# Kernel tuning notes

Hardware: AMD Instinct MI355X
Metric: run time of the kernel (lower is better)

## Reference

```python
import jax, jax.numpy as jnp
import numpy as np

H = 150  # hidden per direction

def _lstm_dir(x, w_ih, w_hh, b_ih, b_hh):
    # x: [B, T, D] -> hs: [B, T, H]; PyTorch gate order i,f,g,o
    B = x.shape[0]
    xg = jnp.einsum('btd,gd->btg', x, w_ih) + b_ih + b_hh  # precompute input projection [B,T,4H]
    def step(carry, xt):
        h, c = carry
        g = xt + h @ w_hh.T
        i, f, gg, o = jnp.split(g, 4, axis=-1)
        i, f, o = jax.nn.sigmoid(i), jax.nn.sigmoid(f), jax.nn.sigmoid(o)
        c = f * c + i * jnp.tanh(gg)
        h = o * jnp.tanh(c)
        return (h, c), h
    init = (jnp.zeros((B, H), x.dtype), jnp.zeros((B, H), x.dtype))
    _, hs = jax.lax.scan(step, init, jnp.swapaxes(xg, 0, 1))  # [T,B,H]
    return jnp.swapaxes(hs, 0, 1)

def _bilstm(x, w_ih_f, w_hh_f, b_ih_f, b_hh_f, w_ih_b, w_hh_b, b_ih_b, b_hh_b):
    fwd = _lstm_dir(x, w_ih_f, w_hh_f, b_ih_f, b_hh_f)
    bwd = jnp.flip(_lstm_dir(jnp.flip(x, axis=1), w_ih_b, w_hh_b, b_ih_b, b_hh_b), axis=1)
    return jnp.concatenate([fwd, bwd], axis=-1)  # [B, T, 2H]

def setup_inputs() -> dict:
    key = jax.random.key(0)
    ks = jax.random.split(key, 20)
    s = 0.05
    d = {
        'sentences': jax.random.normal(ks[0], (1024, 128, 343), jnp.float32),
        'w_ih_f1': jax.random.normal(ks[1], (600, 343)) * s,
        'w_hh_f1': jax.random.normal(ks[2], (600, 150)) * s,
        'b_ih_f1': jax.random.normal(ks[3], (600,)) * s,
        'b_hh_f1': jax.random.normal(ks[4], (600,)) * s,
        'w_ih_b1': jax.random.normal(ks[5], (600, 343)) * s,
        'w_hh_b1': jax.random.normal(ks[6], (600, 150)) * s,
        'b_ih_b1': jax.random.normal(ks[7], (600,)) * s,
        'b_hh_b1': jax.random.normal(ks[8], (600,)) * s,
        'w_ih_f2': jax.random.normal(ks[9], (600, 300)) * s,
        'w_hh_f2': jax.random.normal(ks[10], (600, 150)) * s,
        'b_ih_f2': jax.random.normal(ks[11], (600,)) * s,
        'b_hh_f2': jax.random.normal(ks[12], (600,)) * s,
        'w_ih_b2': jax.random.normal(ks[13], (600, 300)) * s,
        'w_hh_b2': jax.random.normal(ks[14], (600, 150)) * s,
        'b_ih_b2': jax.random.normal(ks[15], (600,)) * s,
        'b_hh_b2': jax.random.normal(ks[16], (600,)) * s,
        'w_out': jax.random.normal(ks[17], (7, 300)) * s,
        'b_out': jax.random.normal(ks[18], (7,)) * s,
    }
    return d

def reference(sentences, w_ih_f1, w_hh_f1, b_ih_f1, b_hh_f1, w_ih_b1, w_hh_b1, b_ih_b1, b_hh_b1,
              w_ih_f2, w_hh_f2, b_ih_f2, b_hh_f2, w_ih_b2, w_hh_b2, b_ih_b2, b_hh_b2, w_out, b_out):
    # Layer 1: per-sentence BiLSTM over words, batched instead of a python loop (dropout is eval-mode identity)
    word_out = _bilstm(sentences, w_ih_f1, w_hh_f1, b_ih_f1, b_hh_f1, w_ih_b1, w_hh_b1, b_ih_b1, b_hh_b1)  # [S,T,300]
    sent_emb = jnp.max(word_out, axis=1)  # max-pool over words -> [S,300]
    # Layer 2: BiLSTM over the sequence of sentence embeddings (batch of 1 paragraph)
    sent_out = _bilstm(sent_emb[None], w_ih_f2, w_hh_f2, b_ih_f2, b_hh_f2, w_ih_b2, w_hh_b2, b_ih_b2, b_hh_b2)[0]  # [S,300]
    log_probs = jax.nn.log_softmax(sent_out @ w_out.T + b_out, axis=-1)  # [S,7]
    return log_probs
```

## Files before the change

kernel.cpp:

```cpp
#include <hip/hip_runtime.h>
#include <hip/hip_bf16.h>
#include <hip/hip_fp16.h>

typedef short bf16x8 __attribute__((ext_vector_type(8)));
typedef float f32x4 __attribute__((ext_vector_type(4)));
typedef unsigned short u16x4 __attribute__((ext_vector_type(4)));
typedef unsigned int uint32;

#define MFMA_B16(a,b,c) __builtin_amdgcn_mfma_f32_16x16x32_bf16(a,b,c,0,0,0)

#define NS   1024
#define TLEN 128
#define DD   343
#define HH   150
#define GG   600
#define KX   352
#define KXP  44
#define KHP  20
#define NP   640

#define OFF_WXP  0u
#define OFF_WHP  901120u
#define OFF_B1   1310720u
#define OFF_W2B  1315840u
#define OFF_W2I  1725440u
#define OFF_SE   3184640u
#define OFF_XG2  4413440u
#define OFF_H2O  9328640u
#define OFF_XBF  10557440u
#define NEED_BF  102832128ull

#define PE0 450560
#define PE1 655360
#define PE2 656640
#define PE3 861440
#define PE4 1226240

__device__ __forceinline__ float rcp_fast(float x) { return __builtin_amdgcn_rcpf(x); }
__device__ __forceinline__ float sigm(float x) { return rcp_fast(1.f + __expf(-x)); }
__device__ __forceinline__ float tanh_fast(float x) { return 1.f - 2.f * rcp_fast(__expf(2.f * x) + 1.f); }

typedef __attribute__((address_space(1))) const void GASV;
typedef __attribute__((address_space(3))) void LASV;
__device__ __forceinline__ void gload_lds16(const void* g, void* l) {
  __builtin_amdgcn_global_load_lds((GASV*)g, (LASV*)l, 16, 0, 0);
}

__device__ __forceinline__ void bar_lds() {
  asm volatile("s_waitcnt lgkmcnt(0)" ::: "memory");
  __builtin_amdgcn_s_barrier();
  asm volatile("" ::: "memory");
}
__device__ __forceinline__ void bar_full() {
  asm volatile("s_waitcnt vmcnt(0) lgkmcnt(0)" ::: "memory");
  __builtin_amdgcn_s_barrier();
  asm volatile("" ::: "memory");
}

__device__ __forceinline__ unsigned short f2bu(float v) {
  __hip_bfloat16 b = __float2bfloat16(v);
  return __builtin_bit_cast(unsigned short, b);
}

__global__ __launch_bounds__(256) void prep_kernel(
    const float* __restrict__ wif1, const float* __restrict__ whf1,
    const float* __restrict__ bif1, const float* __restrict__ bhf1,
    const float* __restrict__ wib1, const float* __restrict__ whb1,
    const float* __restrict__ bib1, const float* __restrict__ bhb1,
    const float* __restrict__ wif2, const float* __restrict__ wib2,
    const float* __restrict__ whf2, const float* __restrict__ whb2,
    __hip_bfloat16* __restrict__ WXp, __hip_bfloat16* __restrict__ WHp,
    float* __restrict__ B1, __hip_bfloat16* __restrict__ W2B, float* __restrict__ W2I)
{
  int i = blockIdx.x * 256 + threadIdx.x;
  if (i < PE0) {
    int d = i / 225280; int r = i - d * 225280;
    int p = r / 5120;   int r2 = r - p * 5120;
    int n = r2 >> 3;    int j = r2 & 7;
    int k = p * 8 + j;
    const float* w = d ? wib1 : wif1;
    float v = (n < GG && k < DD) ? w[n * DD + k] : 0.f;
    WXp[i] = __float2bfloat16(v);
  } else if (i < PE1) {
    int ii = i - PE0;
    int d = ii / 102400; int r = ii - d * 102400;
    int p = r / 5120;    int r2 = r - p * 5120;
    int n = r2 >> 3;     int j = r2 & 7;
    int k = p * 8 + j;
    const float* w = d ? whb1 : whf1;
    float v = (n < GG && k < HH) ? w[n * HH + k] : 0.f;
    WHp[ii] = __float2bfloat16(v);
  } else if (i < PE2) {
    int ii = i - PE1;
    int d = ii / NP; int n = ii - d * NP;
    float v = 0.f;
    if (n < GG) v = d ? (bib1[n] + bhb1[n]) : (bif1[n] + bhf1[n]);
    B1[ii] = v;
  } else if (i < PE3) {
    int ii = i - PE2;
    int d = ii / 102400; int r = ii - d * 102400;
    int n = r / 160;     int k = r - n * 160;
    const float* w = d ? whb2 : whf2;
    float v = (n < GG && k < HH) ? w[n * HH + k] : 0.f;
    W2B[ii] = __float2bfloat16(v);
  } else if (i < PE4) {
    int ii = i - PE3;
    int d = ii / 182400; int r = ii - d * 182400;
    int k = r / 608;     int n = r - k * 608;
    const float* w = d ? wib2 : wif2;
    float v = (n < GG) ? w[n * 300 + k] : 0.f;
    W2I[ii] = v;
  }
}

__global__ __launch_bounds__(256) void xcvt_kernel(
    const float* __restrict__ x, __hip_bfloat16* __restrict__ XBF)
{
  const int total4 = NS * TLEN * (KX / 4);
  for (int idx = blockIdx.x * 256 + threadIdx.x; idx < total4; idx += gridDim.x * 256) {
    int row = idx / 88;
    int c4 = (idx - row * 88) * 4;
    const float* src = x + (size_t)row * DD + c4;
    float v0 = 0.f, v1 = 0.f, v2 = 0.f, v3 = 0.f;
    if (c4 + 3 < DD) {
      v0 = __builtin_nontemporal_load(src);
      v1 = __builtin_nontemporal_load(src + 1);
      v2 = __builtin_nontemporal_load(src + 2);
      v3 = __builtin_nontemporal_load(src + 3);
    } else {
      if (c4 < DD)     v0 = src[0];
      if (c4 + 1 < DD) v1 = src[1];
      if (c4 + 2 < DD) v2 = src[2];
    }
    u16x4 o;
    o.x = f2bu(v0); o.y = f2bu(v1); o.z = f2bu(v2); o.w = f2bu(v3);
    u16x4* dst = (u16x4*)((unsigned short*)XBF + (size_t)row * KX + c4);
    __builtin_nontemporal_store(o, dst);
  }
}

#define XS_SZ   45056u
#define HS_OFF  (2u * XS_SZ)
#define GS_OFF  (HS_OFF + 5120u)
#define CF_OFF  (GS_OFF + 19328u)
#define MX_OFF  (CF_OFF + 4864u)
#define L1_SMEM (MX_OFF + 4864u)

template<bool BF>
__device__ __forceinline__ void stage_x(char* xsd, const float* __restrict__ x,
                                        const __hip_bfloat16* __restrict__ XBF,
                                        int t0, int dir, int s0, int tid, int lane, int wv)
{
  if constexpr (BF) {
    #pragma unroll
    for (int i = 0; i < 6; ++i) {
      int id = i * 8 + wv;
      if (id < 44) {
        int chunk = id * 64 + lane;
        int row16 = chunk / 44;
        int col16 = chunk - row16 * 44;
        int p = row16 >> 4, rr = row16 & 15;
        int t = t0 + 2 * p + (rr >> 3);
        int s = s0 + (rr & 7);
        int tt = dir ? (127 - t) : t;
        const __hip_bfloat16* gp = XBF + ((size_t)s * TLEN + tt) * KX + col16 * 8;
        gload_lds16((const void*)gp, (void*)(xsd + id * 1024));
      }
    }
  } else {
    for (int e = tid; e < 4 * 16 * KX; e += 512) {
      int row16 = e / KX;
      int col = e - row16 * KX;
      int p = row16 >> 4, rr = row16 & 15;
      int t = t0 + 2 * p + (rr >> 3);
      int s = s0 + (rr & 7);
      int tt = dir ? (127 - t) : t;
      float v = (col < DD) ? x[((size_t)s * TLEN + tt) * DD + col] : 0.f;
      ((__hip_bfloat16*)xsd)[e] = __float2bfloat16(v);
    }
  }
}

__device__ __forceinline__ void cell_pass(float* gs, float* cf, float* mx,
                                          __hip_bfloat16* hs, int tid, bool odd)
{
  for (int e = tid; e < 8 * HH; e += 512) {
    int s = e / HH, j = e - s * HH;
    float iv = sigm(gs[s * 604 + j]);
    float fv = sigm(gs[s * 604 + 150 + j]);
    float gv = tanh_fast(gs[s * 604 + 300 + j]);
    float ov = sigm(gs[s * 604 + 450 + j]);
    float c = fv * cf[s * 152 + j] + iv * gv;
    cf[s * 152 + j] = c;
    float h = ov * tanh_fast(c);
    mx[s * 152 + j] = fmaxf(mx[s * 152 + j], h);
    if (odd) {
      hs[s * 160 + j] = __float2bfloat16(h);
      hs[(8 + s) * 160 + j] = __float2bfloat16(0.f);
    } else {
      hs[(8 + s) * 160 + j] = __float2bfloat16(h);
    }
  }
}

template<bool BF>
__global__ __launch_bounds__(512) __attribute__((amdgpu_waves_per_eu(1, 2)))
void lstm1_kernel(
    const float* __restrict__ x, const __hip_bfloat16* __restrict__ XBF,
    const __hip_bfloat16* __restrict__ WXp, const __hip_bfloat16* __restrict__ WHp,
    const float* __restrict__ B1, float* __restrict__ SE)
{
  extern __shared__ char smem[];
  char* xs0 = smem;
  char* xs1 = smem + XS_SZ;
  __hip_bfloat16* hs = (__hip_bfloat16*)(smem + HS_OFF);
  float* gs = (float*)(smem + GS_OFF);
  float* cf = (float*)(smem + CF_OFF);
  float* mx = (float*)(smem + MX_OFF);

  const int tid = threadIdx.x;
  const int lane = tid & 63;
  const int wv = tid >> 6;
  const int dir = blockIdx.x & 1;
  const int s0 = (blockIdx.x >> 1) * 8;
  const int arow = lane & 15;
  const int kgrp = lane >> 4;
  const int nb = wv * 80;

  for (int e = tid; e < 16 * 160; e += 512) hs[e] = __float2bfloat16(0.f);
  for (int e = tid; e < 8 * 152; e += 512) { cf[e] = 0.f; mx[e] = -3e38f; }

  float bias[5];
  #pragma unroll
  for (int nt = 0; nt < 5; ++nt) {
    int n = nb + nt * 16 + arow;
    bias[nt] = (n < GG) ? B1[dir * NP + n] : 0.f;
    asm volatile("" : "+v"(bias[nt]));
  }

  const __hip_bfloat16* WXd = WXp + (size_t)dir * KXP * NP * 8;
  const __hip_bfloat16* WHd = WHp + (size_t)dir * KHP * NP * 8;

  bf16x8 whr[5][5];
  #pragma unroll
  for (int kh = 0; kh < 5; ++kh)
    #pragma unroll
    for (int nt = 0; nt < 5; ++nt)
      whr[kh][nt] = *reinterpret_cast<const bf16x8*>(
          WHd + ((size_t)(kh * 4 + kgrp) * NP + nb + nt * 16 + arow) * 8);
  #pragma unroll
  for (int kh = 0; kh < 5; ++kh)
    #pragma unroll
    for (int nt = 0; nt < 5; ++nt)
      asm volatile("" : "+v"(whr[kh][nt]));

  stage_x<BF>(xs0, x, XBF, 0, dir, s0, tid, lane, wv);
  bar_full();

  for (int g = 0; g < 16; ++g) {
    char* xsc = (g & 1) ? xs1 : xs0;
    char* xsn = (g & 1) ? xs0 : xs1;
    const __hip_bfloat16* xsb = (const __hip_bfloat16*)xsc;

    f32x4 acc[4][5];
    #pragma unroll
    for (int p = 0; p < 4; ++p)
      #pragma unroll
      for (int nt = 0; nt < 5; ++nt) acc[p][nt] = (f32x4){0.f, 0.f, 0.f, 0.f};

    for (int kk = 0; kk < 11; ++kk) {
      bf16x8 a[4], b[5];
      #pragma unroll
      for (int p = 0; p < 4; ++p)
        a[p] = *reinterpret_cast<const bf16x8*>(xsb + (p * 16 + arow) * KX + kk * 32 + kgrp * 8);
      #pragma unroll
      for (int nt = 0; nt < 5; ++nt)
        b[nt] = *reinterpret_cast<const bf16x8*>(
            WXd + ((size_t)(kk * 4 + kgrp) * NP + nb + nt * 16 + arow) * 8);
      #pragma unroll
      for (int p = 0; p < 4; ++p)
        #pragma unroll
        for (int nt = 0; nt < 5; ++nt)
          acc[p][nt] = MFMA_B16(a[p], b[nt], acc[p][nt]);
    }

    if (g < 15)
      stage_x<BF>(xsn, x, XBF, (g + 1) * 8, dir, s0, tid, lane, wv);

    #pragma unroll
    for (int p = 0; p < 4; ++p) {
      #pragma unroll
      for (int kh = 0; kh < 5; ++kh) {
        bf16x8 ah = *reinterpret_cast<const bf16x8*>(hs + arow * 160 + kh * 32 + kgrp * 8);
        #pragma unroll
        for (int nt = 0; nt < 5; ++nt)
          acc[p][nt] = MFMA_B16(ah, whr[kh][nt], acc[p][nt]);
      }
      if (kgrp < 2) {
        #pragma unroll
        for (int nt = 0; nt < 5; ++nt) {
          int n = nb + nt * 16 + arow;
          if (n < GG) {
            #pragma unroll
            for (int r = 0; r < 4; ++r)
              gs[(kgrp * 4 + r) * 604 + n] = acc[p][nt][r] + bias[nt];
          }
        }
      }
      bar_lds();
      cell_pass(gs, cf, mx, hs, tid, false);
      bar_lds();
      #pragma unroll
      for (int kh = 0; kh < 5; ++kh) {
        bf16x8 ah = *reinterpret_cast<const bf16x8*>(hs + arow * 160 + kh * 32 + kgrp * 8);
        #pragma unroll
        for (int nt = 0; nt < 5; ++nt)
          acc[p][nt] = MFMA_B16(ah, whr[kh][nt], acc[p][nt]);
      }
      if (kgrp >= 2) {
        #pragma unroll
        for (int nt = 0; nt < 5; ++nt) {
          int n = nb + nt * 16 + arow;
          if (n < GG) {
            #pragma unroll
            for (int r = 0; r < 4; ++r)
              gs[((kgrp - 2) * 4 + r) * 604 + n] = acc[p][nt][r] + bias[nt];
          }
        }
      }
      bar_lds();
      cell_pass(gs, cf, mx, hs, tid, true);
      if (p == 3) bar_full(); else bar_lds();
    }
  }

  for (int e = tid; e < 8 * HH; e += 512) {
    int s = e / HH, j = e - s * HH;
    SE[(size_t)(s0 + s) * 300 + dir * HH + j] = mx[s * 152 + j];
  }
}

__global__ __launch_bounds__(256, 1) void xg2_kernel(
    const float* __restrict__ SE, const float* __restrict__ W2I,
    const float* __restrict__ bif2, const float* __restrict__ bhf2,
    const float* __restrict__ bib2, const float* __restrict__ bhb2,
    float* __restrict__ XG2)
{
  __shared__ float se[32 * 304];
  const int d = blockIdx.x >> 5, st = blockIdx.x & 31, sb = st * 32;
  const int tid = threadIdx.x;
  for (int e = tid; e < 32 * 300; e += 256) {
    int si = e / 300, k = e - si * 300;
    se[si * 304 + k] = SE[(size_t)(sb + si) * 300 + k];
  }
  __syncthreads();
  for (int pass = 0; pass < 3; ++pass) {
    int n = pass * 256 + tid;
    if (n < GG) {
      float bias = d ? (bib2[n] + bhb2[n]) : (bif2[n] + bhf2[n]);
      float acc[32];
      #pragma unroll
      for (int si = 0; si < 32; ++si) acc[si] = bias;
      const float* wcol = W2I + (size_t)d * 300 * 608 + n;
      for (int k = 0; k < 300; ++k) {
        float wvv = wcol[(size_t)k * 608];
        #pragma unroll
        for (int si = 0; si < 32; ++si) acc[si] += wvv * se[si * 304 + k];
      }
      #pragma unroll
      for (int si = 0; si < 32; ++si)
        XG2[((size_t)d * NS + sb + si) * GG + n] = acc[si];
    }
  }
}

__global__ __launch_bounds__(640) __attribute__((amdgpu_waves_per_eu(1, 3)))
void lstm2_kernel(
    const __hip_bfloat16* __restrict__ W2B, const float* __restrict__ XG2,
    float* __restrict__ H2O)
{
  const int dir = blockIdx.x;
  const int tid = threadIdx.x;
  const int lane = tid & 63;
  const int wv = tid >> 6;
  const int c16 = lane & 15;
  const int kg = lane >> 4;
  __shared__ float gls[NP];
  __shared__ __align__(16) __hip_bfloat16 hbuf[160];

  const __hip_bfloat16* Wd = W2B + (size_t)dir * NP * 160;
  bf16x8 wf[5][4];
  #pragma unroll
  for (int kt = 0; kt < 5; ++kt)
    #pragma unroll
    for (int nt = 0; nt < 4; ++nt)
      wf[kt][nt] = *reinterpret_cast<const bf16x8*>(
          Wd + (size_t)(wv * 64 + nt * 16 + c16) * 160 + kt * 32 + kg * 8);

  if (tid < 160) hbuf[tid] = __float2bfloat16(0.f);
  __syncthreads();

  float creg = 0.f;
  const float* xg = XG2 + (size_t)dir * NS * GG;
  const int gcol = (tid < GG) ? tid : (GG - 1);
  const bool isg = (tid >= 300) && (tid < 450);
  float xnext = xg[(size_t)(dir ? 1023 : 0) * GG + gcol];

  for (int step = 0; step < 1024; ++step) {
    const int ss = dir ? (1023 - step) : step;
    float xn = 0.f;
    if (step < 1023) {
      int ss2 = dir ? (1022 - step) : (step + 1);
      xn = xg[(size_t)ss2 * GG + gcol];
    }
    bf16x8 hf[5];
    #pragma unroll
    for (int kt = 0; kt < 5; ++kt)
      hf[kt] = *reinterpret_cast<const bf16x8*>(hbuf + kt * 32 + kg * 8);
    f32x4 a0 = {0.f,0.f,0.f,0.f}, a1 = {0.f,0.f,0.f,0.f};
    f32x4 a2 = {0.f,0.f,0.f,0.f}, a3 = {0.f,0.f,0.f,0.f};
    #pragma unroll
    for (int kt = 0; kt < 5; ++kt) {
      a0 = MFMA_B16(hf[kt], wf[kt][0], a0);
      a1 = MFMA_B16(hf[kt], wf[kt][1], a1);
      a2 = MFMA_B16(hf[kt], wf[kt][2], a2);
      a3 = MFMA_B16(hf[kt], wf[kt][3], a3);
    }
    float y = (kg == 0) ? a0[0] : (kg == 1) ? a1[0] : (kg == 2) ? a2[0] : a3[0];
    float acc = y + xnext;
    gls[tid] = isg ? tanh_fast(acc) : sigm(acc);
    bar_lds();
    if (tid < HH) {
      float iv = gls[tid], fv = gls[150 + tid], gv = gls[300 + tid], ov = gls[450 + tid];
      creg = fv * creg + iv * gv;
      float nh = ov * tanh_fast(creg);
      H2O[(size_t)ss * 300 + dir * HH + tid] = nh;
      hbuf[tid] = __float2bfloat16(nh);
    }
    bar_lds();
    xnext = xn;
  }
}

__global__ __launch_bounds__(256, 1) void head_kernel(
    const float* __restrict__ H2O, const float* __restrict__ w_out,
    const float* __restrict__ b_out, float* __restrict__ out)
{
  int s = blockIdx.x * 256 + threadIdx.x;
  if (s >= NS) return;
  float acc[7];
  #pragma unroll
  for (int c = 0; c < 7; ++c) acc[c] = b_out[c];
  const float* hrow = H2O + (size_t)s * 300;
  for (int k = 0; k < 300; ++k) {
    float hv = hrow[k];
    #pragma unroll
    for (int c = 0; c < 7; ++c) acc[c] += hv * w_out[c * 300 + k];
  }
  float m = acc[0];
  #pragma unroll
  for (int c = 1; c < 7; ++c) m = fmaxf(m, acc[c]);
  float sum = 0.f;
  #pragma unroll
  for (int c = 0; c < 7; ++c) sum += __expf(acc[c] - m);
  float lse = m + __logf(sum);
  #pragma unroll
  for (int c = 0; c < 7; ++c) out[s * 7 + c] = acc[c] - lse;
}

extern "C" void kernel_launch(void* const* d_in, const int* in_sizes, int n_in,
                              void* d_out, int out_size, void* d_ws, size_t ws_size,
                              hipStream_t stream) {
  const float* x      = (const float*)d_in[0];
  const float* wif1   = (const float*)d_in[1];
  const float* whf1   = (const float*)d_in[2];
  const float* bif1   = (const float*)d_in[3];
  const float* bhf1   = (const float*)d_in[4];
  const float* wib1   = (const float*)d_in[5];
  const float* whb1   = (const float*)d_in[6];
  const float* bib1   = (const float*)d_in[7];
  const float* bhb1   = (const float*)d_in[8];
  const float* wif2   = (const float*)d_in[9];
  const float* whf2   = (const float*)d_in[10];
  const float* bif2   = (const float*)d_in[11];
  const float* bhf2   = (const float*)d_in[12];
  const float* wib2   = (const float*)d_in[13];
  const float* whb2   = (const float*)d_in[14];
  const float* bib2   = (const float*)d_in[15];
  const float* bhb2   = (const float*)d_in[16];
  const float* w_out  = (const float*)d_in[17];
  const float* b_out  = (const float*)d_in[18];

  char* ws = (char*)d_ws;
  __hip_bfloat16* WXp = (__hip_bfloat16*)(ws + OFF_WXP);
  __hip_bfloat16* WHp = (__hip_bfloat16*)(ws + OFF_WHP);
  float*    B1  = (float*)(ws + OFF_B1);
  __hip_bfloat16* W2B = (__hip_bfloat16*)(ws + OFF_W2B);
  float*    W2I = (float*)(ws + OFF_W2I);
  float*    SE  = (float*)(ws + OFF_SE);
  float*    XG2 = (float*)(ws + OFF_XG2);
  float*    H2O = (float*)(ws + OFF_H2O);
  __hip_bfloat16* XBF = (__hip_bfloat16*)(ws + OFF_XBF);

  const bool useBF = (ws_size >= NEED_BF);

  prep_kernel<<<(PE4 + 255) / 256, 256, 0, stream>>>(
      wif1, whf1, bif1, bhf1, wib1, whb1, bib1, bhb1,
      wif2, wib2, whf2, whb2, WXp, WHp, B1, W2B, W2I);

  if (useBF)
    xcvt_kernel<<<4096, 256, 0, stream>>>(x, XBF);

  (void)hipFuncSetAttribute((const void*)(lstm1_kernel<true>),
                            hipFuncAttributeMaxDynamicSharedMemorySize, L1_SMEM);
  (void)hipFuncSetAttribute((const void*)(lstm1_kernel<false>),
                            hipFuncAttributeMaxDynamicSharedMemorySize, L1_SMEM);

  if (useBF)
    lstm1_kernel<true><<<256, 512, L1_SMEM, stream>>>(x, XBF, WXp, WHp, B1, SE);
  else
    lstm1_kernel<false><<<256, 512, L1_SMEM, stream>>>(x, XBF, WXp, WHp, B1, SE);

  xg2_kernel<<<64, 256, 0, stream>>>(SE, W2I, bif2, bhf2, bib2, bhb2, XG2);

  lstm2_kernel<<<2, 640, 0, stream>>>(W2B, XG2, H2O);

  head_kernel<<<4, 256, 0, stream>>>(H2O, w_out, b_out, (float*)d_out);
}
```

Before: 1.593 ms.

## Gate-interleave weight layout so LSTM cell math runs in MFMA registers

Weights, biases and the layer-2 input projection are repacked so the four gates for hidden unit j sit at columns g*160+j. Each lane then holds all four gate pre-activations for its unit and applies the cell update directly in registers. This drops the LDS gate buffer, the separate cell_pass loop and one barrier per half-step in layer 1, and in layer 2 it removes the gate exchange through shared memory. In exchange, layer-1 blocks grow to 640 threads with a 4-timestep tile, which halves the x-projection tile per pass and doubles the outer iterations; a dummy 102400-byte dynamic LDS request is added, and layer 2 gains a double-buffered h.

```diff
diff --git a/kernel.cpp b/kernel.cpp
--- a/kernel.cpp
+++ b/kernel.cpp
@@ -16,8 +16,8 @@
 #define GG   600
 #define KX   352
 #define KXP  44
-#define KHP  20
 #define NP   640
+#define NG2  640
 
 #define OFF_WXP  0u
 #define OFF_WHP  901120u
@@ -26,9 +26,9 @@
 #define OFF_W2I  1725440u
 #define OFF_SE   3184640u
 #define OFF_XG2  4413440u
-#define OFF_H2O  9328640u
-#define OFF_XBF  10557440u
-#define NEED_BF  102832128ull
+#define OFF_H2O  9656320u
+#define OFF_XBF  10885120u
+#define NEED_BF  103159808ull
 
 #define PE0 450560
 #define PE1 655360
@@ -76,32 +76,39 @@
   if (i < PE0) {
     int d = i / 225280; int r = i - d * 225280;
     int p = r / 5120;   int r2 = r - p * 5120;
-    int n = r2 >> 3;    int j = r2 & 7;
-    int k = p * 8 + j;
+    int n2 = r2 >> 3;   int jj = r2 & 7;
+    int k = p * 8 + jj;
+    int g = n2 / 160, j = n2 - g * 160;
     const float* w = d ? wib1 : wif1;
-    float v = (n < GG && k < DD) ? w[n * DD + k] : 0.f;
+    float v = (j < HH && k < DD) ? w[(g * HH + j) * DD + k] : 0.f;
     WXp[i] = __float2bfloat16(v);
   } else if (i < PE1) {
     int ii = i - PE0;
     int d = ii / 102400; int r = ii - d * 102400;
     int p = r / 5120;    int r2 = r - p * 5120;
-    int n = r2 >> 3;     int j = r2 & 7;
-    int k = p * 8 + j;
+    int n2 = r2 >> 3;    int jj = r2 & 7;
+    int k = p * 8 + jj;
+    int g = n2 / 160, j = n2 - g * 160;
     const float* w = d ? whb1 : whf1;
-    float v = (n < GG && k < HH) ? w[n * HH + k] : 0.f;
+    float v = (j < HH && k < HH) ? w[(g * HH + j) * HH + k] : 0.f;
     WHp[ii] = __float2bfloat16(v);
   } else if (i < PE2) {
     int ii = i - PE1;
-    int d = ii / NP; int n = ii - d * NP;
+    int d = ii / NP; int n2 = ii - d * NP;
+    int g = n2 / 160, j = n2 - g * 160;
     float v = 0.f;
-    if (n < GG) v = d ? (bib1[n] + bhb1[n]) : (bif1[n] + bhf1[n]);
+    if (j < HH) {
+      int n = g * HH + j;
+      v = d ? (bib1[n] + bhb1[n]) : (bif1[n] + bhf1[n]);
+    }
     B1[ii] = v;
   } else if (i < PE3) {
     int ii = i - PE2;
     int d = ii / 102400; int r = ii - d * 102400;
-    int n = r / 160;     int k = r - n * 160;
+    int n2 = r / 160;    int k = r - n2 * 160;
+    int g = n2 / 160, j = n2 - g * 160;
     const float* w = d ? whb2 : whf2;
-    float v = (n < GG && k < HH) ? w[n * HH + k] : 0.f;
+    float v = (j < HH && k < HH) ? w[(g * HH + j) * HH + k] : 0.f;
     W2B[ii] = __float2bfloat16(v);
   } else if (i < PE4) {
     int ii = i - PE3;
@@ -139,12 +146,10 @@
   }
 }
 
-#define XS_SZ   45056u
+#define XS_SZ   22528u
 #define HS_OFF  (2u * XS_SZ)
-#define GS_OFF  (HS_OFF + 5120u)
-#define CF_OFF  (GS_OFF + 19328u)
-#define MX_OFF  (CF_OFF + 4864u)
-#define L1_SMEM (MX_OFF + 4864u)
+#define L1_SMEM (HS_OFF + 5120u)
+#define L1_SMEM_REQ 102400u
 
 template<bool BF>
 __device__ __forceinline__ void stage_x(char* xsd, const float* __restrict__ x,
@@ -153,9 +158,9 @@
 {
   if constexpr (BF) {
     #pragma unroll
-    for (int i = 0; i < 6; ++i) {
-      int id = i * 8 + wv;
-      if (id < 44) {
+    for (int i = 0; i < 3; ++i) {
+      int id = i * 10 + wv;
+      if (id < 22) {
         int chunk = id * 64 + lane;
         int row16 = chunk / 44;
         int col16 = chunk - row16 * 44;
@@ -168,7 +173,7 @@
       }
     }
   } else {
-    for (int e = tid; e < 4 * 16 * KX; e += 512) {
+    for (int e = tid; e < 2 * 16 * KX; e += 640) {
       int row16 = e / KX;
       int col = e - row16 * KX;
       int p = row16 >> 4, rr = row16 & 15;
@@ -181,30 +186,8 @@
   }
 }
 
-__device__ __forceinline__ void cell_pass(float* gs, float* cf, float* mx,
-                                          __hip_bfloat16* hs, int tid, bool odd)
-{
-  for (int e = tid; e < 8 * HH; e += 512) {
-    int s = e / HH, j = e - s * HH;
-    float iv = sigm(gs[s * 604 + j]);
-    float fv = sigm(gs[s * 604 + 150 + j]);
-    float gv = tanh_fast(gs[s * 604 + 300 + j]);
-    float ov = sigm(gs[s * 604 + 450 + j]);
-    float c = fv * cf[s * 152 + j] + iv * gv;
-    cf[s * 152 + j] = c;
-    float h = ov * tanh_fast(c);
-    mx[s * 152 + j] = fmaxf(mx[s * 152 + j], h);
-    if (odd) {
-      hs[s * 160 + j] = __float2bfloat16(h);
-      hs[(8 + s) * 160 + j] = __float2bfloat16(0.f);
-    } else {
-      hs[(8 + s) * 160 + j] = __float2bfloat16(h);
-    }
-  }
-}
-
 template<bool BF>
-__global__ __launch_bounds__(512) __attribute__((amdgpu_waves_per_eu(1, 2)))
+__global__ __launch_bounds__(640)
 void lstm1_kernel(
     const float* __restrict__ x, const __hip_bfloat16* __restrict__ XBF,
     const __hip_bfloat16* __restrict__ WXp, const __hip_bfloat16* __restrict__ WHp,
@@ -214,129 +197,136 @@
   char* xs0 = smem;
   char* xs1 = smem + XS_SZ;
   __hip_bfloat16* hs = (__hip_bfloat16*)(smem + HS_OFF);
-  float* gs = (float*)(smem + GS_OFF);
-  float* cf = (float*)(smem + CF_OFF);
-  float* mx = (float*)(smem + MX_OFF);
 
   const int tid = threadIdx.x;
   const int lane = tid & 63;
   const int wv = tid >> 6;
   const int dir = blockIdx.x & 1;
   const int s0 = (blockIdx.x >> 1) * 8;
-  const int arow = lane & 15;
+  const int c16 = lane & 15;
   const int kgrp = lane >> 4;
-  const int nb = wv * 80;
-
-  for (int e = tid; e < 16 * 160; e += 512) hs[e] = __float2bfloat16(0.f);
-  for (int e = tid; e < 8 * 152; e += 512) { cf[e] = 0.f; mx[e] = -3e38f; }
-
-  float bias[5];
-  #pragma unroll
-  for (int nt = 0; nt < 5; ++nt) {
-    int n = nb + nt * 16 + arow;
-    bias[nt] = (n < GG) ? B1[dir * NP + n] : 0.f;
-    asm volatile("" : "+v"(bias[nt]));
+  const int j = wv * 16 + c16;
+
+  for (int e = tid; e < 16 * 160; e += 640) hs[e] = __float2bfloat16(0.f);
+
+  float bias[4];
+  #pragma unroll
+  for (int g4 = 0; g4 < 4; ++g4) {
+    bias[g4] = B1[dir * NP + g4 * 160 + j];
+    asm volatile("" : "+v"(bias[g4]));
   }
 
   const __hip_bfloat16* WXd = WXp + (size_t)dir * KXP * NP * 8;
-  const __hip_bfloat16* WHd = WHp + (size_t)dir * KHP * NP * 8;
-
-  bf16x8 whr[5][5];
+  const __hip_bfloat16* WHd = WHp + (size_t)dir * 20 * NP * 8;
+
+  bf16x8 whr[5][4];
   #pragma unroll
   for (int kh = 0; kh < 5; ++kh)
     #pragma unroll
-    for (int nt = 0; nt < 5; ++nt)
-      whr[kh][nt] = *reinterpret_cast<const bf16x8*>(
-          WHd + ((size_t)(kh * 4 + kgrp) * NP + nb + nt * 16 + arow) * 8);
-  #pragma unroll
-  for (int kh = 0; kh < 5; ++kh)
-    #pragma unroll
-    for (int nt = 0; nt < 5; ++nt)
-      asm volatile("" : "+v"(whr[kh][nt]));
+    for (int g4 = 0; g4 < 4; ++g4) {
+      whr[kh][g4] = *reinterpret_cast<const bf16x8*>(
+          WHd + ((size_t)(kh * 4 + kgrp) * NP + g4 * 160 + j) * 8);
+      asm volatile("" : "+v"(whr[kh][g4]));
+    }
+
+  float creg[4] = {0.f, 0.f, 0.f, 0.f};
+  float mxr[4] = {-3e38f, -3e38f, -3e38f, -3e38f};
 
   stage_x<BF>(xs0, x, XBF, 0, dir, s0, tid, lane, wv);
   bar_full();
 
-  for (int g = 0; g < 16; ++g) {
+  for (int g = 0; g < 32; ++g) {
     char* xsc = (g & 1) ? xs1 : xs0;
     char* xsn = (g & 1) ? xs0 : xs1;
     const __hip_bfloat16* xsb = (const __hip_bfloat16*)xsc;
 
-    f32x4 acc[4][5];
-    #pragma unroll
-    for (int p = 0; p < 4; ++p)
-      #pragma unroll
-      for (int nt = 0; nt < 5; ++nt) acc[p][nt] = (f32x4){0.f, 0.f, 0.f, 0.f};
+    f32x4 acc[2][4];
+    #pragma unroll
+    for (int p = 0; p < 2; ++p)
+      #pragma unroll
+      for (int g4 = 0; g4 < 4; ++g4) acc[p][g4] = (f32x4){0.f, 0.f, 0.f, 0.f};
 
     for (int kk = 0; kk < 11; ++kk) {
-      bf16x8 a[4], b[5];
-      #pragma unroll
-      for (int p = 0; p < 4; ++p)
-        a[p] = *reinterpret_cast<const bf16x8*>(xsb + (p * 16 + arow) * KX + kk * 32 + kgrp * 8);
-      #pragma unroll
-      for (int nt = 0; nt < 5; ++nt)
-        b[nt] = *reinterpret_cast<const bf16x8*>(
-            WXd + ((size_t)(kk * 4 + kgrp) * NP + nb + nt * 16 + arow) * 8);
-      #pragma unroll
-      for (int p = 0; p < 4; ++p)
+      bf16x8 a[2], b[4];
+      #pragma unroll
+      for (int p = 0; p < 2; ++p)
+        a[p] = *reinterpret_cast<const bf16x8*>(xsb + (p * 16 + c16) * KX + kk * 32 + kgrp * 8);
+      #pragma unroll
+      for (int g4 = 0; g4 < 4; ++g4)
+        b[g4] = *reinterpret_cast<const bf16x8*>(
+            WXd + ((size_t)(kk * 4 + kgrp) * NP + g4 * 160 + j) * 8);
+      #pragma unroll
+      for (int p = 0; p < 2; ++p)
         #pragma unroll
-        for (int nt = 0; nt < 5; ++nt)
-          acc[p][nt] = MFMA_B16(a[p], b[nt], acc[p][nt]);
-    }
-
-    if (g < 15)
-      stage_x<BF>(xsn, x, XBF, (g + 1) * 8, dir, s0, tid, lane, wv);
-
-    #pragma unroll
-    for (int p = 0; p < 4; ++p) {
+        for (int g4 = 0; g4 < 4; ++g4)
+          acc[p][g4] = MFMA_B16(a[p], b[g4], acc[p][g4]);
+    }
+
+    if (g < 31)
+      stage_x<BF>(xsn, x, XBF, (g + 1) * 4, dir, s0, tid, lane, wv);
+
+    #pragma unroll
+    for (int p = 0; p < 2; ++p) {
       #pragma unroll
       for (int kh = 0; kh < 5; ++kh) {
-        bf16x8 ah = *reinterpret_cast<const bf16x8*>(hs + arow * 160 + kh * 32 + kgrp * 8);
+        bf16x8 ah = *reinterpret_cast<const bf16x8*>(hs + c16 * 160 + kh * 32 + kgrp * 8);
         #pragma unroll
-        for (int nt = 0; nt < 5; ++nt)
-          acc[p][nt] = MFMA_B16(ah, whr[kh][nt], acc[p][nt]);
+        for (int g4 = 0; g4 < 4; ++g4)
+          acc[p][g4] = MFMA_B16(ah, whr[kh][g4], acc[p][g4]);
       }
-      if (kgrp < 2) {
+      {
+        const bool act = (kgrp < 2);
         #pragma unroll
-        for (int nt = 0; nt < 5; ++nt) {
-          int n = nb + nt * 16 + arow;
-          if (n < GG) {
-            #pragma unroll
-            for (int r = 0; r < 4; ++r)
-              gs[(kgrp * 4 + r) * 604 + n] = acc[p][nt][r] + bias[nt];
+        for (int r = 0; r < 4; ++r) {
+          float iv = sigm(acc[p][0][r] + bias[0]);
+          float fv = sigm(acc[p][1][r] + bias[1]);
+          float gv = tanh_fast(acc[p][2][r] + bias[2]);
+          float ov = sigm(acc[p][3][r] + bias[3]);
+          float cin = __shfl_xor(creg[r], 32);
+          float cn = fv * cin + iv * gv;
+          float h = ov * tanh_fast(cn);
+          creg[r] = act ? cn : creg[r];
+          mxr[r] = act ? fmaxf(mxr[r], h) : mxr[r];
+          if (act) hs[(8 + kgrp * 4 + r) * 160 + j] = __float2bfloat16(h);
+        }
+      }
+      bar_lds();
+      #pragma unroll
+      for (int kh = 0; kh < 5; ++kh) {
+        bf16x8 ah = *reinterpret_cast<const bf16x8*>(hs + c16 * 160 + kh * 32 + kgrp * 8);
+        #pragma unroll
+        for (int g4 = 0; g4 < 4; ++g4)
+          acc[p][g4] = MFMA_B16(ah, whr[kh][g4], acc[p][g4]);
+      }
+      {
+        const bool act = (kgrp >= 2);
+        #pragma unroll
+        for (int r = 0; r < 4; ++r) {
+          float iv = sigm(acc[p][0][r] + bias[0]);
+          float fv = sigm(acc[p][1][r] + bias[1]);
+          float gv = tanh_fast(acc[p][2][r] + bias[2]);
+          float ov = sigm(acc[p][3][r] + bias[3]);
+          float cin = __shfl_xor(creg[r], 32);
+          float cn = fv * cin + iv * gv;
+          float h = ov * tanh_fast(cn);
+          creg[r] = act ? cn : creg[r];
+          mxr[r] = act ? fmaxf(mxr[r], h) : mxr[r];
+          if (act) {
+            int s = (kgrp - 2) * 4 + r;
+            hs[s * 160 + j] = __float2bfloat16(h);
+            hs[(8 + s) * 160 + j] = __float2bfloat16(0.f);
           }
         }
       }
-      bar_lds();
-      cell_pass(gs, cf, mx, hs, tid, false);
-      bar_lds();
-      #pragma unroll
-      for (int kh = 0; kh < 5; ++kh) {
-        bf16x8 ah = *reinterpret_cast<const bf16x8*>(hs + arow * 160 + kh * 32 + kgrp * 8);
-        #pragma unroll
-        for (int nt = 0; nt < 5; ++nt)
-          acc[p][nt] = MFMA_B16(ah, whr[kh][nt], acc[p][nt]);
-      }
-      if (kgrp >= 2) {
-        #pragma unroll
-        for (int nt = 0; nt < 5; ++nt) {
-          int n = nb + nt * 16 + arow;
-          if (n < GG) {
-            #pragma unroll
-            for (int r = 0; r < 4; ++r)
-              gs[((kgrp - 2) * 4 + r) * 604 + n] = acc[p][nt][r] + bias[nt];
-          }
-        }
-      }
-      bar_lds();
-      cell_pass(gs, cf, mx, hs, tid, true);
-      if (p == 3) bar_full(); else bar_lds();
-    }
-  }
-
-  for (int e = tid; e < 8 * HH; e += 512) {
-    int s = e / HH, j = e - s * HH;
-    SE[(size_t)(s0 + s) * 300 + dir * HH + j] = mx[s * 152 + j];
+      if (p == 1) bar_full(); else bar_lds();
+    }
+  }
+
+  #pragma unroll
+  for (int r = 0; r < 4; ++r) {
+    float m = fmaxf(mxr[r], __shfl_xor(mxr[r], 32));
+    if (kgrp < 2 && j < HH)
+      SE[(size_t)(s0 + kgrp * 4 + r) * 300 + dir * HH + j] = m;
   }
 }
 
@@ -357,6 +347,7 @@
   for (int pass = 0; pass < 3; ++pass) {
     int n = pass * 256 + tid;
     if (n < GG) {
+      int n2 = (n / 150) * 160 + (n % 150);
       float bias = d ? (bib2[n] + bhb2[n]) : (bif2[n] + bhf2[n]);
       float acc[32];
       #pragma unroll
@@ -369,13 +360,17 @@
       }
       #pragma unroll
       for (int si = 0; si < 32; ++si)
-        XG2[((size_t)d * NS + sb + si) * GG + n] = acc[si];
-    }
-  }
-}
-
-__global__ __launch_bounds__(640) __attribute__((amdgpu_waves_per_eu(1, 3)))
-void lstm2_kernel(
+        XG2[((size_t)d * NS + sb + si) * NG2 + n2] = acc[si];
+    }
+  }
+  for (int e = tid; e < 32 * 40; e += 256) {
+    int si = e / 40, q = e - si * 40;
+    int g = q / 10, jp = 150 + (q - g * 10);
+    XG2[((size_t)d * NS + sb + si) * NG2 + g * 160 + jp] = 0.f;
+  }
+}
+
+__global__ __launch_bounds__(640) void lstm2_kernel(
     const __hip_bfloat16* __restrict__ W2B, const float* __restrict__ XG2,
     float* __restrict__ H2O)
 {
@@ -385,60 +380,72 @@
   const int wv = tid >> 6;
   const int c16 = lane & 15;
   const int kg = lane >> 4;
-  __shared__ float gls[NP];
-  __shared__ __align__(16) __hip_bfloat16 hbuf[160];
+  const int j = wv * 16 + c16;
+  __shared__ __align__(16) __hip_bfloat16 hbuf[2][160];
+
+  const f32x4 ZERO4 = {0.f, 0.f, 0.f, 0.f};
 
   const __hip_bfloat16* Wd = W2B + (size_t)dir * NP * 160;
   bf16x8 wf[5][4];
   #pragma unroll
   for (int kt = 0; kt < 5; ++kt)
     #pragma unroll
-    for (int nt = 0; nt < 4; ++nt)
-      wf[kt][nt] = *reinterpret_cast<const bf16x8*>(
-          Wd + (size_t)(wv * 64 + nt * 16 + c16) * 160 + kt * 32 + kg * 8);
-
-  if (tid < 160) hbuf[tid] = __float2bfloat16(0.f);
+    for (int g4 = 0; g4 < 4; ++g4) {
+      wf[kt][g4] = *reinterpret_cast<const bf16x8*>(
+          Wd + (size_t)(g4 * 160 + j) * 160 + kt * 32 + kg * 8);
+      asm volatile("" : "+v"(wf[kt][g4]));
+    }
+
+  if (tid < 160) hbuf[0][tid] = __float2bfloat16(0.f);
   __syncthreads();
 
   float creg = 0.f;
-  const float* xg = XG2 + (size_t)dir * NS * GG;
-  const int gcol = (tid < GG) ? tid : (GG - 1);
-  const bool isg = (tid >= 300) && (tid < 450);
-  float xnext = xg[(size_t)(dir ? 1023 : 0) * GG + gcol];
+  const float* xg = XG2 + (size_t)dir * NS * NG2;
+  float xv[4];
+  {
+    int ss0 = dir ? 1023 : 0;
+    #pragma unroll
+    for (int g4 = 0; g4 < 4; ++g4) xv[g4] = xg[(size_t)ss0 * NG2 + g4 * 160 + j];
+  }
 
   for (int step = 0; step < 1024; ++step) {
     const int ss = dir ? (1023 - step) : step;
-    float xn = 0.f;
+    float xn[4] = {0.f, 0.f, 0.f, 0.f};
     if (step < 1023) {
       int ss2 = dir ? (1022 - step) : (step + 1);
-      xn = xg[(size_t)ss2 * GG + gcol];
-    }
+      #pragma unroll
+      for (int g4 = 0; g4 < 4; ++g4) xn[g4] = xg[(size_t)ss2 * NG2 + g4 * 160 + j];
+    }
+    const int cur = step & 1;
     bf16x8 hf[5];
     #pragma unroll
     for (int kt = 0; kt < 5; ++kt)
-      hf[kt] = *reinterpret_cast<const bf16x8*>(hbuf + kt * 32 + kg * 8);
-    f32x4 a0 = {0.f,0.f,0.f,0.f}, a1 = {0.f,0.f,0.f,0.f};
-    f32x4 a2 = {0.f,0.f,0.f,0.f}, a3 = {0.f,0.f,0.f,0.f};
-    #pragma unroll
-    for (int kt = 0; kt < 5; ++kt) {
-      a0 = MFMA_B16(hf[kt], wf[kt][0], a0);
-      a1 = MFMA_B16(hf[kt], wf[kt][1], a1);
-      a2 = MFMA_B16(hf[kt], wf[kt][2], a2);
-      a3 = MFMA_B16(hf[kt], wf[kt][3], a3);
-    }
-    float y = (kg == 0) ? a0[0] : (kg == 1) ? a1[0] : (kg == 2) ? a2[0] : a3[0];
-    float acc = y + xnext;
-    gls[tid] = isg ? tanh_fast(acc) : sigm(acc);
+      hf[kt] = *reinterpret_cast<const bf16x8*>(&hbuf[cur][kt * 32 + kg * 8]);
+    f32x4 aA[4], aB[4];
+    #pragma unroll
+    for (int g4 = 0; g4 < 4; ++g4) {
+      aA[g4] = MFMA_B16(hf[0], wf[0][g4], ZERO4);
+      aB[g4] = MFMA_B16(hf[1], wf[1][g4], ZERO4);
+    }
+    #pragma unroll
+    for (int g4 = 0; g4 < 4; ++g4) {
+      aA[g4] = MFMA_B16(hf[2], wf[2][g4], aA[g4]);
+      aB[g4] = MFMA_B16(hf[3], wf[3][g4], aB[g4]);
+      aA[g4] = MFMA_B16(hf[4], wf[4][g4], aA[g4]);
+    }
+    float iv = sigm(aA[0][0] + aB[0][0] + xv[0]);
+    float fv = sigm(aA[1][0] + aB[1][0] + xv[1]);
+    float gv = tanh_fast(aA[2][0] + aB[2][0] + xv[2]);
+    float ov = sigm(aA[3][0] + aB[3][0] + xv[3]);
+    creg = fv * creg + iv * gv;
+    float nh = ov * tanh_fast(creg);
+    if (kg == 0) {
+      hbuf[cur ^ 1][j] = __float2bfloat16(nh);
+      if (j < HH) H2O[(size_t)ss * 300 + dir * HH + j] = nh;
+    }
     bar_lds();
-    if (tid < HH) {
-      float iv = gls[tid], fv = gls[150 + tid], gv = gls[300 + tid], ov = gls[450 + tid];
-      creg = fv * creg + iv * gv;
-      float nh = ov * tanh_fast(creg);
-      H2O[(size_t)ss * 300 + dir * HH + tid] = nh;
-      hbuf[tid] = __float2bfloat16(nh);
-    }
-    bar_lds();
-    xnext = xn;
+    #pragma unroll
+    for (int g4 = 0; g4 < 4; ++g4) xv[g4] = xn[g4];
   }
 }
 
@@ -512,14 +519,14 @@
     xcvt_kernel<<<4096, 256, 0, stream>>>(x, XBF);
 
   (void)hipFuncSetAttribute((const void*)(lstm1_kernel<true>),
-                            hipFuncAttributeMaxDynamicSharedMemorySize, L1_SMEM);
+                            hipFuncAttributeMaxDynamicSharedMemorySize, L1_SMEM_REQ);
   (void)hipFuncSetAttribute((const void*)(lstm1_kernel<false>),
-                            hipFuncAttributeMaxDynamicSharedMemorySize, L1_SMEM);
+                            hipFuncAttributeMaxDynamicSharedMemorySize, L1_SMEM_REQ);
 
   if (useBF)
-    lstm1_kernel<true><<<256, 512, L1_SMEM, stream>>>(x, XBF, WXp, WHp, B1, SE);
+    lstm1_kernel<true><<<256, 640, L1_SMEM_REQ, stream>>>(x, XBF, WXp, WHp, B1, SE);
   else
-    lstm1_kernel<false><<<256, 512, L1_SMEM, stream>>>(x, XBF, WXp, WHp, B1, SE);
+    lstm1_kernel<false><<<256, 640, L1_SMEM_REQ, stream>>>(x, XBF, WXp, WHp, B1, SE);
 
   xg2_kernel<<<64, 256, 0, stream>>>(SE, W2I, bif2, bhf2, bib2, bhb2, XG2);
 
```

New measurement: 1.726 ms. 1.08x slower.
